# Kernel tuning notes

Hardware: AMD Instinct MI355X
Metric: run time of the kernel (lower is better)

Reference implementation:

```python
import jax, jax.numpy as jnp
import numpy as np

N = 50000
E = 800000
IN, HID, OUT = 256, 128, 128
H = 2


def gat_conv(x, edge_src, edge_dst, W, att_src, att_dst, bias, concat=True):
    # PyG GATConv: x' = W x, edge attention e = leaky_relu(a_s.x'_src + a_d.x'_dst),
    # softmax over incoming edges of each dst node, weighted scatter-add.
    n = x.shape[0]
    heads, ch = att_src.shape
    xl = (x @ W).reshape(n, heads, ch)                      # [N,H,C]
    a_src = jnp.sum(xl * att_src[None], axis=-1)            # [N,H]
    a_dst = jnp.sum(xl * att_dst[None], axis=-1)            # [N,H]
    e = a_src[edge_src] + a_dst[edge_dst]                   # [E,H]
    e = jax.nn.leaky_relu(e, negative_slope=0.2)
    # segment softmax over dst neighborhoods (self-loops guarantee non-empty)
    emax = jax.ops.segment_max(e, edge_dst, num_segments=n)
    ee = jnp.exp(e - emax[edge_dst])
    denom = jax.ops.segment_sum(ee, edge_dst, num_segments=n)
    alpha = ee / (denom[edge_dst] + 1e-16)                  # [E,H]
    msg = xl[edge_src] * alpha[:, :, None]                  # [E,H,C]
    out = jax.ops.segment_sum(msg, edge_dst, num_segments=n)  # [N,H,C]
    out = out.reshape(n, heads * ch) if concat else out.mean(axis=1)
    return out + bias


def setup_inputs() -> dict:
    key = jax.random.key(0)
    ks = jax.random.split(key, 12)
    x = jax.random.normal(ks[0], (N, IN), dtype=jnp.float32)
    edge_index = jax.random.randint(ks[1], (2, E), 0, N, dtype=jnp.int64)
    node_type = (jnp.arange(N, dtype=jnp.int64) % 3)
    agent_idx = jnp.arange(0, N, 3, dtype=jnp.int64)  # nodes with type 0
    # layer 0: in=256 -> out=128, heads=2, concat
    W0 = jax.random.normal(ks[2], (IN, H * HID), dtype=jnp.float32) / np.sqrt(IN)
    as0 = jax.random.normal(ks[3], (H, HID), dtype=jnp.float32) / np.sqrt(HID)
    ad0 = jax.random.normal(ks[4], (H, HID), dtype=jnp.float32) / np.sqrt(HID)
    b0 = jnp.zeros((H * HID,), dtype=jnp.float32)
    # layer 1: in=128*2 -> out=128, heads=2, concat (average_last=False)
    W1 = jax.random.normal(ks[5], (H * HID, H * OUT), dtype=jnp.float32) / np.sqrt(H * HID)
    as1 = jax.random.normal(ks[6], (H, OUT), dtype=jnp.float32) / np.sqrt(OUT)
    ad1 = jax.random.normal(ks[7], (H, OUT), dtype=jnp.float32) / np.sqrt(OUT)
    b1 = jnp.zeros((H * OUT,), dtype=jnp.float32)
    return {"x": x, "edge_index": edge_index, "node_type": node_type,
            "agent_idx": agent_idx, "W0": W0, "as0": as0, "ad0": ad0, "b0": b0,
            "W1": W1, "as1": as1, "ad1": ad1, "b1": b1}


def reference(x, edge_index, node_type, agent_idx, W0, as0, ad0, b0, W1, as1, ad1, b1):
    # add self loops (PyG GATConv default add_self_loops=True)
    loop = jnp.arange(N, dtype=edge_index.dtype)
    src = jnp.concatenate([edge_index[0], loop])
    dst = jnp.concatenate([edge_index[1], loop])
    final = []
    h = gat_conv(x, src, dst, W0, as0, ad0, b0, concat=True)
    h = jax.nn.sigmoid(h)
    final.append(h[agent_idx])  # full_receptive_field=True
    h = gat_conv(h, src, dst, W1, as1, ad1, b1, concat=True)
    h = jax.nn.sigmoid(h)
    final.append(h[agent_idx])
    return jnp.concatenate(final, axis=1)  # [n_agents, 128*2 + 128*2]
```

## Files before the change

kernel.cpp:

```cpp
#include <hip/hip_runtime.h>
#include <hip/hip_fp16.h>

typedef unsigned short u16;
typedef unsigned int   u32;
typedef unsigned char  u8;
typedef __attribute__((ext_vector_type(8))) short short8;
typedef __attribute__((ext_vector_type(8))) unsigned short ushort8v;
typedef __attribute__((ext_vector_type(4))) float f32x4;

#define TPB 256

#define GLDS16(g,l) __builtin_amdgcn_global_load_lds( \
    (const __attribute__((address_space(1))) void*)(g), \
    (__attribute__((address_space(3))) void*)(l), 16, 0, 0)

__device__ __forceinline__ float b2f(u16 u){ u32 x=((u32)u)<<16; return __uint_as_float(x); }
__device__ __forceinline__ u16 f2b(float f){ u32 x=__float_as_uint(f); u32 r=x+0x7FFFu+((x>>16)&1u); return (u16)(r>>16); }
__device__ __forceinline__ float lrelu(float x){ return x>0.f?x:0.2f*x; }
__device__ __forceinline__ float sigm(float x){ return 1.f/(1.f+__expf(-x)); }

__device__ __forceinline__ float4 ld4(const void* p, size_t i4, int isbf){
  if(isbf){
    ushort4 u=((const ushort4*)p)[i4];
    return make_float4(b2f(u.x),b2f(u.y),b2f(u.z),b2f(u.w));
  }
  return ((const float4*)p)[i4];
}
__device__ __forceinline__ float ld1(const void* p, size_t i, int isbf){
  return isbf ? b2f(((const u16*)p)[i]) : ((const float*)p)[i];
}

__global__ void k_deg(const int* __restrict__ dst, int E, int N, int* __restrict__ deg,
                      int* __restrict__ pos,
                      int* __restrict__ ainv, const u16* __restrict__ w0, int* __restrict__ flag){
  int gid=blockIdx.x*blockDim.x+threadIdx.x;
  if(blockIdx.x==0){
    __shared__ int s[256];
    int t=threadIdx.x, sane=0;
    for(int i=t;i<512;i+=256){
      u16 u=w0[i]; u32 e=(u>>7)&0xFFu;
      if((e>=103u&&e<=143u)||((u&0x7FFFu)==0u)) sane++;
    }
    s[t]=sane; __syncthreads();
    for(int o=128;o;o>>=1){ if(t<o) s[t]+=s[t+o]; __syncthreads(); }
    if(t==0) flag[0]=(s[0]>=480)?1:0;
  }
  if(gid<N) ainv[gid]=-1;
  if(gid>=E+N) return;
  int d=(gid<E)?dst[gid]:(gid-E);
  d=min(max(d,0),N-1);
  pos[gid]=atomicAdd(&deg[d],1);
}

__global__ void k_scan(const int* __restrict__ deg, int* __restrict__ rs,
                       int* __restrict__ counter, int n,
                       const int* __restrict__ aidx, int* __restrict__ ainv, int na){
  __shared__ int tmp[TPB];
  __shared__ int base;
  int i=blockIdx.x*TPB+threadIdx.x;
  if(i<na){ int a=aidx[i]; if(a>=0&&a<n) ainv[a]=i; }
  int v=(i<n)?deg[i]:0;
  tmp[threadIdx.x]=v; __syncthreads();
  for(int off=1;off<TPB;off<<=1){
    int t=(threadIdx.x>=off)?tmp[threadIdx.x-off]:0;
    __syncthreads();
    tmp[threadIdx.x]+=t;
    __syncthreads();
  }
  if(threadIdx.x==TPB-1) base=atomicAdd(counter,tmp[TPB-1]);
  __syncthreads();
  if(i<n) rs[i]=base+tmp[threadIdx.x]-v;
}

__global__ void k_fill(const int* __restrict__ src, const int* __restrict__ dst, int E, int N,
                       const int* __restrict__ rs, const int* __restrict__ pos,
                       int* __restrict__ col){
  int e=blockIdx.x*blockDim.x+threadIdx.x; if(e>=E+N) return;
  int d,s;
  if(e<E){ d=dst[e]; s=src[e]; } else { d=e-E; s=e-E; }
  d=min(max(d,0),N-1); s=min(max(s,0),N-1);
  col[rs[d]+pos[e]]=s;
}

__global__ __launch_bounds__(256) void k_prep(const void* __restrict__ Wa, u16* __restrict__ WTa,
                                              const void* __restrict__ Wb, u16* __restrict__ WTb,
                                              const void* __restrict__ X, u16* __restrict__ xb,
                                              int n8, const int* __restrict__ flag){
  const int isbf=flag[0];
  int bid=blockIdx.x;
  if(bid<32){
    __shared__ float s[64][65];
    int z=bid>>4, y=(bid>>2)&3, xb_=bid&3;
    const void* W = z ? Wb : Wa;
    u16* WT = z ? WTb : WTa;
    int tx=threadIdx.x&63, ty=threadIdx.x>>6;
    int k0=xb_*64, n0=y*64;
    #pragma unroll
    for(int i=0;i<64;i+=4)
      s[ty+i][tx]=ld1(W,(size_t)(k0+ty+i)*256+n0+tx,isbf);
    __syncthreads();
    #pragma unroll
    for(int i=0;i<64;i+=4)
      WT[(size_t)(n0+ty+i)*256+k0+tx]=f2b(s[tx][ty+i]);
    return;
  }
  int i=(bid-32)*256+threadIdx.x; if(i>=n8) return;
  size_t e=(size_t)i*8;
  if(isbf){
    *(ushort8v*)(xb+e)=*(const ushort8v*)((const u16*)X+e);
  }else{
    const float4* fp=(const float4*)((const float*)X+e);
    float4 f0=fp[0], f1=fp[1];
    ushort8v o;
    o[0]=f2b(f0.x); o[1]=f2b(f0.y); o[2]=f2b(f0.z); o[3]=f2b(f0.w);
    o[4]=f2b(f1.x); o[5]=f2b(f1.y); o[6]=f2b(f1.z); o[7]=f2b(f1.w);
    *(ushort8v*)(xb+e)=o;
  }
}

__global__ __launch_bounds__(256) void k_gemm(const u16* __restrict__ A, const u16* __restrict__ BT,
                                              u16* __restrict__ C, int M){
  __shared__ short As[128*64];
  __shared__ short Bs[128*64];
  const int t=threadIdx.x;
  const int lane=t&63, wv=t>>6;
  const int wm=wv>>1, wn=wv&1;
  const int m15=lane&15, kg=lane>>4;
  const int gm0=blockIdx.x*128, n0=blockIdx.y*128;
  const int sr=lane>>3, slot=lane&7;
  f32x4 acc[4][4]={};
  for(int k0=0;k0<256;k0+=64){
    #pragma unroll
    for(int i=0;i<4;++i){
      int r=wv*32+i*8+sr;
      int kq=slot^(r&7);
      int ga=gm0+r; ga=ga<M?ga:M-1;
      GLDS16(A+(size_t)ga*256+k0+kq*8, As+(wv*32+i*8)*64);
      GLDS16(BT+(size_t)(n0+r)*256+k0+kq*8, Bs+(wv*32+i*8)*64);
    }
    __syncthreads();
    #pragma unroll
    for(int s=0;s<2;++s){
      short8 af[4], bf[4];
      #pragma unroll
      for(int mi=0;mi<4;++mi){
        int row=wm*64+mi*16+m15;
        int sl=(s*4+kg)^(row&7);
        af[mi]=*(const short8*)&As[row*64+sl*8];
      }
      #pragma unroll
      for(int ni=0;ni<4;++ni){
        int row=wn*64+ni*16+m15;
        int sl=(s*4+kg)^(row&7);
        bf[ni]=*(const short8*)&Bs[row*64+sl*8];
      }
      #pragma unroll
      for(int mi=0;mi<4;++mi)
        #pragma unroll
        for(int ni=0;ni<4;++ni)
          acc[mi][ni]=__builtin_amdgcn_mfma_f32_16x16x32_bf16(af[mi],bf[ni],acc[mi][ni],0,0,0);
    }
    __syncthreads();
  }
  #pragma unroll
  for(int mi=0;mi<4;++mi){
    #pragma unroll
    for(int r=0;r<4;++r){
      int grow=gm0+wm*64+mi*16+kg*4+r;
      if(grow<M){
        #pragma unroll
        for(int ni=0;ni<4;++ni){
          int gcol=n0+wn*64+ni*16+m15;
          C[(size_t)grow*256+gcol]=f2b(acc[mi][ni][r]);
        }
      }
    }
  }
}

__global__ __launch_bounds__(256) void k_att(const u16* __restrict__ xl, const void* __restrict__ as_,
                                             const void* __restrict__ ad_, float4* __restrict__ asv,
                                             float2* __restrict__ adv, u8* __restrict__ xl8,
                                             int n, const int* __restrict__ flag){
  const int isbf=flag[0];
  int w=(blockIdx.x*256+threadIdx.x)>>6;
  int lane=threadIdx.x&63;
  if(w>=n) return;
  int ch=lane*4;
  ushort4 u=*(const ushort4*)(xl+(size_t)w*256+ch);
  float4 s=ld4(as_,ch>>2,isbf);
  float4 d=ld4(ad_,ch>>2,isbf);
  float x0=b2f(u.x),x1=b2f(u.y),x2=b2f(u.z),x3=b2f(u.w);
  float m=fmaxf(fmaxf(fabsf(x0),fabsf(x1)),fmaxf(fabsf(x2),fabsf(x3)));
  for(int off=32;off;off>>=1) m=fmaxf(m,__shfl_xor(m,off));
  float mm=fmaxf(m,1e-20f);
  float scale=mm*(1.f/127.f);
  float rsc=127.f/mm;
  int q0=(int)rintf(fmaf(x0,rsc,128.f));
  int q1=(int)rintf(fmaf(x1,rsc,128.f));
  int q2=(int)rintf(fmaf(x2,rsc,128.f));
  int q3=(int)rintf(fmaf(x3,rsc,128.f));
  u32 pack=(u32)q0|((u32)q1<<8)|((u32)q2<<16)|((u32)q3<<24);
  ((u32*)(xl8+(size_t)w*256))[lane]=pack;
  float ps=x0*s.x+x1*s.y+x2*s.z+x3*s.w;
  float pd=x0*d.x+x1*d.y+x2*d.z+x3*d.w;
  for(int off=16;off;off>>=1){ ps+=__shfl_xor(ps,off); pd+=__shfl_xor(pd,off); }
  float ps1=__shfl(ps,32), pd1=__shfl(pd,32);
  if(lane==0){
    asv[w]=make_float4(ps,ps1,scale,0.f);
    adv[w]=make_float2(pd,pd1);
  }
}

__global__ __launch_bounds__(256) void k_alpha(const int* __restrict__ rs, const int* __restrict__ deg,
    const int* __restrict__ col, const float4* __restrict__ asv, const float2* __restrict__ adv,
    int2* __restrict__ ew, float2* __restrict__ rden, int n){
  int w=(blockIdx.x*256+threadIdx.x)>>5;
  int lane=threadIdx.x&31;
  if(w>=n) return;
  int s0=rs[w], cnt=deg[w];
  float2 ad=adv[w];
  float sum0=0.f, sum1=0.f;
  for(int base=0;base<cnt;base+=32){
    int j=base+lane;
    if(j<cnt){
      int sv=col[s0+j];
      float4 a=asv[sv];
      float e0=fminf(lrelu(a.x+ad.x),11.f);
      float e1=fminf(lrelu(a.y+ad.y),11.f);
      float w0=__expf(e0), w1=__expf(e1);
      sum0+=w0; sum1+=w1;
      __half2 p=__floats2half2_rn(w0*a.z,w1*a.z);
      ew[s0+j]=make_int2(sv,*(int*)&p);
    }
  }
  for(int off=16;off;off>>=1){ sum0+=__shfl_xor(sum0,off); sum1+=__shfl_xor(sum1,off); }
  if(lane==0) rden[w]=make_float2(1.f/(sum0+1e-16f),1.f/(sum1+1e-16f));
}

__global__ __launch_bounds__(256) void k_agg(const int* __restrict__ rs, const int* __restrict__ deg,
    const int2* __restrict__ ew, const float2* __restrict__ rden,
    const u8* __restrict__ xl8, const void* __restrict__ bias,
    u16* __restrict__ hout, void* __restrict__ out, int ostride, int ocol,
    const int* __restrict__ ainv, int n, const int* __restrict__ flag){
  const int isbf=flag[0];
  int w=(blockIdx.x*blockDim.x+threadIdx.x)>>5;
  int sl=threadIdx.x&31;
  if(w>=n) return;
  int s0=rs[w], cnt=deg[w];
  int ch=sl*8, h=sl>>4;
  float acc[8]={};
  float sumw=0.f;
  int2 eA[4]; uint2 rA[4];
  int2 eB[4]; uint2 rB[4];
#define LOADG(e_,r_,J) do{ \
    _Pragma("unroll") \
    for(int u=0;u<4;++u){ int idx=(J)+u; idx=idx<cnt?idx:cnt-1; e_[u]=ew[s0+idx]; } \
    _Pragma("unroll") \
    for(int u=0;u<4;++u) r_[u]=*(const uint2*)(xl8+(size_t)e_[u].x*256+ch); \
  }while(0)
#define COMPG(e_,r_,J) do{ \
    _Pragma("unroll") \
    for(int u=0;u<4;++u){ \
      __half2 p=*(__half2*)&e_[u].y; \
      float wb=__half2float(h?__high2half(p):__low2half(p)); \
      wb=((J)+u<cnt)?wb:0.f; \
      u32 a=r_[u].x, b=r_[u].y; \
      acc[0]=fmaf(wb,(float)( a     &255u),acc[0]); \
      acc[1]=fmaf(wb,(float)((a>> 8)&255u),acc[1]); \
      acc[2]=fmaf(wb,(float)((a>>16)&255u),acc[2]); \
      acc[3]=fmaf(wb,(float)( a>>24      ),acc[3]); \
      acc[4]=fmaf(wb,(float)( b     &255u),acc[4]); \
      acc[5]=fmaf(wb,(float)((b>> 8)&255u),acc[5]); \
      acc[6]=fmaf(wb,(float)((b>>16)&255u),acc[6]); \
      acc[7]=fmaf(wb,(float)( b>>24      ),acc[7]); \
      sumw+=wb; \
    } \
  }while(0)
  LOADG(eA,rA,0);
  int j=0;
  while(j<cnt){
    LOADG(eB,rB,j+4);
    COMPG(eA,rA,j);
    j+=4;
    if(j>=cnt) break;
    LOADG(eA,rA,j+4);
    COMPG(eB,rB,j);
    j+=4;
  }
#undef LOADG
#undef COMPG
  float2 rd=rden[w];
  float rh=h?rd.y:rd.x;
  float4 b0=ld4(bias,ch>>2,isbf);
  float4 b1=ld4(bias,(ch>>2)+1,isbf);
  float c=128.f*sumw;
  float r[8];
  r[0]=sigm((acc[0]-c)*rh+b0.x); r[1]=sigm((acc[1]-c)*rh+b0.y);
  r[2]=sigm((acc[2]-c)*rh+b0.z); r[3]=sigm((acc[3]-c)*rh+b0.w);
  r[4]=sigm((acc[4]-c)*rh+b1.x); r[5]=sigm((acc[5]-c)*rh+b1.y);
  r[6]=sigm((acc[6]-c)*rh+b1.z); r[7]=sigm((acc[7]-c)*rh+b1.w);
  ushort8v ov;
  #pragma unroll
  for(int q=0;q<8;++q) ov[q]=f2b(r[q]);
  if(hout) *(ushort8v*)(hout+(size_t)w*256+ch)=ov;
  int ar=ainv[w];
  if(ar>=0){
    size_t o=(size_t)ar*ostride+ocol+ch;
    if(isbf){
      *(ushort8v*)((u16*)out+o)=ov;
    }else{
      *(float4*)((float*)out+o)  =make_float4(r[0],r[1],r[2],r[3]);
      *(float4*)((float*)out+o+4)=make_float4(r[4],r[5],r[6],r[7]);
    }
  }
}

extern "C" void kernel_launch(void* const* d_in, const int* in_sizes, int n_in,
                              void* d_out, int out_size, void* d_ws, size_t ws_size,
                              hipStream_t stream) {
  const void* x   = d_in[0];
  const int*  ei  = (const int*)d_in[1];
  const int*  aidx= (const int*)d_in[3];
  const void* W0  = d_in[4];
  const void* as0 = d_in[5];
  const void* ad0 = d_in[6];
  const void* b0  = d_in[7];
  const void* W1  = d_in[8];
  const void* as1 = d_in[9];
  const void* ad1 = d_in[10];
  const void* b1  = d_in[11];

  const int N  = in_sizes[0]/256;
  const int E  = in_sizes[1]/2;
  const int na = in_sizes[3];
  const int Et = E+N;

  char* ws=(char*)d_ws; size_t off=0;
  auto alloc=[&](size_t bytes)->void*{ void* p=ws+off; off+=(bytes+255)&~(size_t)255; return p; };
  int*   flg =(int*) alloc(256);
  u16*   xl  =(u16*) alloc((size_t)N*256*2);
  u16*   h1  =(u16*) alloc((size_t)N*256*2);
  u8*    xl8 =(u8*)  alloc((size_t)N*256);
  u16*   WT0 =(u16*) alloc((size_t)256*256*2);
  u16*   WT1 =(u16*) alloc((size_t)256*256*2);
  float4* asv=(float4*)alloc((size_t)N*16);
  float2* adv=(float2*)alloc((size_t)N*8);
  char*  zbase=ws+off;
  int*   deg =(int*) alloc((size_t)N*4);
  int*   ctr =(int*) alloc(256);
  size_t zlen=(ws+off)-zbase;
  int*   pos =(int*) alloc((size_t)Et*4);
  int*   rstp=(int*) alloc((size_t)N*4);
  int*   ainv=(int*) alloc((size_t)N*4);
  int*   col =(int*) alloc((size_t)Et*4);
  int2*  ew  =(int2*)alloc((size_t)Et*8);
  float2* rdn=(float2*)alloc((size_t)N*8);

  u16* xb = h1;

  const int* esrc=ei;
  const int* edst=ei+E;

  hipMemsetAsync(zbase,0,zlen,stream);

  k_deg  <<<(Et+255)/256,256,0,stream>>>(edst,E,N,deg,pos,ainv,(const u16*)W0,flg);
  k_scan <<<(N+TPB-1)/TPB,TPB,0,stream>>>(deg,rstp,ctr,N,aidx,ainv,na);
  k_fill <<<(Et+255)/256,256,0,stream>>>(esrc,edst,E,N,rstp,pos,col);
  k_prep <<<32+(N*32+255)/256,256,0,stream>>>(W0,WT0,W1,WT1,x,xb,N*32,flg);

  dim3 gg((N+127)/128,2);
  k_gemm <<<gg,256,0,stream>>>(xb,WT0,xl,N);
  k_att  <<<(N+3)/4,256,0,stream>>>(xl,as0,ad0,asv,adv,xl8,N,flg);
  k_alpha<<<(N+7)/8,256,0,stream>>>(rstp,deg,col,asv,adv,ew,rdn,N);
  k_agg  <<<(N+7)/8,256,0,stream>>>(rstp,deg,ew,rdn,xl8,b0,h1,d_out,512,0,ainv,N,flg);
  k_gemm <<<gg,256,0,stream>>>(h1,WT1,xl,N);
  k_att  <<<(N+3)/4,256,0,stream>>>(xl,as1,ad1,asv,adv,xl8,N,flg);
  k_alpha<<<(N+7)/8,256,0,stream>>>(rstp,deg,col,asv,adv,ew,rdn,N);
  k_agg  <<<(N+7)/8,256,0,stream>>>(rstp,deg,ew,rdn,xl8,b1,(u16*)nullptr,d_out,512,256,ainv,N,flg);
}
```

Baseline: 339.6 us.

## Merge independent setup kernels into shared launches to cut launch count

Combines the degree-count kernel with the weight-transpose/x-conversion prep into one launch, with prep blocks recomputing the dtype sanity flag locally instead of reading it from global memory. It also merges the CSR fill with the first-layer GEMM into one launch, splitting the work by block index. This removes two kernel launches and lets independent work overlap on the GPU. In exchange the combined kernels carry the larger shared-memory footprint and register pressure of their heaviest branch, and the prep blocks repeat the sanity reduction.

```diff
diff --git a/kernel.cpp b/kernel.cpp
--- a/kernel.cpp
+++ b/kernel.cpp
@@ -30,26 +30,73 @@
   return isbf ? b2f(((const u16*)p)[i]) : ((const float*)p)[i];
 }
 
-__global__ void k_deg(const int* __restrict__ dst, int E, int N, int* __restrict__ deg,
-                      int* __restrict__ pos,
-                      int* __restrict__ ainv, const u16* __restrict__ w0, int* __restrict__ flag){
-  int gid=blockIdx.x*blockDim.x+threadIdx.x;
-  if(blockIdx.x==0){
-    __shared__ int s[256];
-    int t=threadIdx.x, sane=0;
+__global__ __launch_bounds__(256) void k_build(const int* __restrict__ dst, int E, int N,
+    int* __restrict__ deg, int* __restrict__ pos, int* __restrict__ ainv,
+    const u16* __restrict__ w0, int* __restrict__ flag,
+    const void* __restrict__ Wa, u16* __restrict__ WTa,
+    const void* __restrict__ Wb, u16* __restrict__ WTb,
+    const void* __restrict__ X, u16* __restrict__ xb, int n8, int D){
+  __shared__ int sd[256];
+  __shared__ float ts[64][65];
+  int bid=blockIdx.x, t=threadIdx.x;
+  if(bid<D){
+    int gid=bid*256+t;
+    if(bid==0){
+      int sane=0;
+      for(int i=t;i<512;i+=256){
+        u16 u=w0[i]; u32 e2=(u>>7)&0xFFu;
+        if((e2>=103u&&e2<=143u)||((u&0x7FFFu)==0u)) sane++;
+      }
+      sd[t]=sane; __syncthreads();
+      for(int o=128;o;o>>=1){ if(t<o) sd[t]+=sd[t+o]; __syncthreads(); }
+      if(t==0) flag[0]=(sd[0]>=480)?1:0;
+    }
+    if(gid<N) ainv[gid]=-1;
+    if(gid>=E+N) return;
+    int d=(gid<E)?dst[gid]:(gid-E);
+    d=min(max(d,0),N-1);
+    pos[gid]=atomicAdd(&deg[d],1);
+    return;
+  }
+  {
+    int sane=0;
     for(int i=t;i<512;i+=256){
-      u16 u=w0[i]; u32 e=(u>>7)&0xFFu;
-      if((e>=103u&&e<=143u)||((u&0x7FFFu)==0u)) sane++;
-    }
-    s[t]=sane; __syncthreads();
-    for(int o=128;o;o>>=1){ if(t<o) s[t]+=s[t+o]; __syncthreads(); }
-    if(t==0) flag[0]=(s[0]>=480)?1:0;
-  }
-  if(gid<N) ainv[gid]=-1;
-  if(gid>=E+N) return;
-  int d=(gid<E)?dst[gid]:(gid-E);
-  d=min(max(d,0),N-1);
-  pos[gid]=atomicAdd(&deg[d],1);
+      u16 u=w0[i]; u32 e2=(u>>7)&0xFFu;
+      if((e2>=103u&&e2<=143u)||((u&0x7FFFu)==0u)) sane++;
+    }
+    sd[t]=sane; __syncthreads();
+    for(int o=128;o;o>>=1){ if(t<o) sd[t]+=sd[t+o]; __syncthreads(); }
+  }
+  const int isbf=(sd[0]>=480)?1:0;
+  __syncthreads();
+  int pbid=bid-D;
+  if(pbid<32){
+    int z=pbid>>4, y=(pbid>>2)&3, xq=pbid&3;
+    const void* W = z ? Wb : Wa;
+    u16* WT = z ? WTb : WTa;
+    int tx=t&63, ty=t>>6;
+    int k0=xq*64, n0=y*64;
+    #pragma unroll
+    for(int i=0;i<64;i+=4)
+      ts[ty+i][tx]=ld1(W,(size_t)(k0+ty+i)*256+n0+tx,isbf);
+    __syncthreads();
+    #pragma unroll
+    for(int i=0;i<64;i+=4)
+      WT[(size_t)(n0+ty+i)*256+k0+tx]=f2b(ts[tx][ty+i]);
+    return;
+  }
+  int i=(pbid-32)*256+t; if(i>=n8) return;
+  size_t e=(size_t)i*8;
+  if(isbf){
+    *(ushort8v*)(xb+e)=*(const ushort8v*)((const u16*)X+e);
+  }else{
+    const float4* fp=(const float4*)((const float*)X+e);
+    float4 f0=fp[0], f1=fp[1];
+    ushort8v o;
+    o[0]=f2b(f0.x); o[1]=f2b(f0.y); o[2]=f2b(f0.z); o[3]=f2b(f0.w);
+    o[4]=f2b(f1.x); o[5]=f2b(f1.y); o[6]=f2b(f1.z); o[7]=f2b(f1.w);
+    *(ushort8v*)(xb+e)=o;
+  }
 }
 
 __global__ void k_scan(const int* __restrict__ deg, int* __restrict__ rs,
@@ -72,49 +119,74 @@
   if(i<n) rs[i]=base+tmp[threadIdx.x]-v;
 }
 
-__global__ void k_fill(const int* __restrict__ src, const int* __restrict__ dst, int E, int N,
-                       const int* __restrict__ rs, const int* __restrict__ pos,
-                       int* __restrict__ col){
-  int e=blockIdx.x*blockDim.x+threadIdx.x; if(e>=E+N) return;
-  int d,s;
-  if(e<E){ d=dst[e]; s=src[e]; } else { d=e-E; s=e-E; }
-  d=min(max(d,0),N-1); s=min(max(s,0),N-1);
-  col[rs[d]+pos[e]]=s;
-}
-
-__global__ __launch_bounds__(256) void k_prep(const void* __restrict__ Wa, u16* __restrict__ WTa,
-                                              const void* __restrict__ Wb, u16* __restrict__ WTb,
-                                              const void* __restrict__ X, u16* __restrict__ xb,
-                                              int n8, const int* __restrict__ flag){
-  const int isbf=flag[0];
+__global__ __launch_bounds__(256) void k_fillgemm(
+    const int* __restrict__ src, const int* __restrict__ dstp, int E, int N,
+    const int* __restrict__ rs, const int* __restrict__ pos, int* __restrict__ col,
+    const u16* __restrict__ A, const u16* __restrict__ BT, u16* __restrict__ C, int M, int G){
+  __shared__ short As[128*64];
+  __shared__ short Bs[128*64];
   int bid=blockIdx.x;
-  if(bid<32){
-    __shared__ float s[64][65];
-    int z=bid>>4, y=(bid>>2)&3, xb_=bid&3;
-    const void* W = z ? Wb : Wa;
-    u16* WT = z ? WTb : WTa;
-    int tx=threadIdx.x&63, ty=threadIdx.x>>6;
-    int k0=xb_*64, n0=y*64;
-    #pragma unroll
-    for(int i=0;i<64;i+=4)
-      s[ty+i][tx]=ld1(W,(size_t)(k0+ty+i)*256+n0+tx,isbf);
-    __syncthreads();
-    #pragma unroll
-    for(int i=0;i<64;i+=4)
-      WT[(size_t)(n0+ty+i)*256+k0+tx]=f2b(s[tx][ty+i]);
+  const int t=threadIdx.x;
+  if(bid>=G){
+    int e=(bid-G)*256+t; if(e>=E+N) return;
+    int d,s;
+    if(e<E){ d=dstp[e]; s=src[e]; } else { d=e-E; s=e-E; }
+    d=min(max(d,0),N-1); s=min(max(s,0),N-1);
+    col[rs[d]+pos[e]]=s;
     return;
   }
-  int i=(bid-32)*256+threadIdx.x; if(i>=n8) return;
-  size_t e=(size_t)i*8;
-  if(isbf){
-    *(ushort8v*)(xb+e)=*(const ushort8v*)((const u16*)X+e);
-  }else{
-    const float4* fp=(const float4*)((const float*)X+e);
-    float4 f0=fp[0], f1=fp[1];
-    ushort8v o;
-    o[0]=f2b(f0.x); o[1]=f2b(f0.y); o[2]=f2b(f0.z); o[3]=f2b(f0.w);
-    o[4]=f2b(f1.x); o[5]=f2b(f1.y); o[6]=f2b(f1.z); o[7]=f2b(f1.w);
-    *(ushort8v*)(xb+e)=o;
+  const int lane=t&63, wv=t>>6;
+  const int wm=wv>>1, wn=wv&1;
+  const int m15=lane&15, kg=lane>>4;
+  const int gm0=(bid>>1)*128, n0=(bid&1)*128;
+  const int sr=lane>>3, slot=lane&7;
+  f32x4 acc[4][4]={};
+  for(int k0=0;k0<256;k0+=64){
+    #pragma unroll
+    for(int i=0;i<4;++i){
+      int r=wv*32+i*8+sr;
+      int kq=slot^(r&7);
+      int ga=gm0+r; ga=ga<M?ga:M-1;
+      GLDS16(A+(size_t)ga*256+k0+kq*8, As+(wv*32+i*8)*64);
+      GLDS16(BT+(size_t)(n0+r)*256+k0+kq*8, Bs+(wv*32+i*8)*64);
+    }
+    __syncthreads();
+    #pragma unroll
+    for(int s=0;s<2;++s){
+      short8 af[4], bf[4];
+      #pragma unroll
+      for(int mi=0;mi<4;++mi){
+        int row=wm*64+mi*16+m15;
+        int sl=(s*4+kg)^(row&7);
+        af[mi]=*(const short8*)&As[row*64+sl*8];
+      }
+      #pragma unroll
+      for(int ni=0;ni<4;++ni){
+        int row=wn*64+ni*16+m15;
+        int sl=(s*4+kg)^(row&7);
+        bf[ni]=*(const short8*)&Bs[row*64+sl*8];
+      }
+      #pragma unroll
+      for(int mi=0;mi<4;++mi)
+        #pragma unroll
+        for(int ni=0;ni<4;++ni)
+          acc[mi][ni]=__builtin_amdgcn_mfma_f32_16x16x32_bf16(af[mi],bf[ni],acc[mi][ni],0,0,0);
+    }
+    __syncthreads();
+  }
+  #pragma unroll
+  for(int mi=0;mi<4;++mi){
+    #pragma unroll
+    for(int r=0;r<4;++r){
+      int grow=gm0+wm*64+mi*16+kg*4+r;
+      if(grow<M){
+        #pragma unroll
+        for(int ni=0;ni<4;++ni){
+          int gcol=n0+wn*64+ni*16+m15;
+          C[(size_t)grow*256+gcol]=f2b(acc[mi][ni][r]);
+        }
+      }
+    }
   }
 }
 
@@ -364,16 +436,19 @@
 
   hipMemsetAsync(zbase,0,zlen,stream);
 
-  k_deg  <<<(Et+255)/256,256,0,stream>>>(edst,E,N,deg,pos,ainv,(const u16*)W0,flg);
+  const int D = (Et+255)/256;
+  const int P = 32+(N*32+255)/256;
+  k_build<<<D+P,256,0,stream>>>(edst,E,N,deg,pos,ainv,(const u16*)W0,flg,
+                                W0,WT0,W1,WT1,x,xb,N*32,D);
   k_scan <<<(N+TPB-1)/TPB,TPB,0,stream>>>(deg,rstp,ctr,N,aidx,ainv,na);
-  k_fill <<<(Et+255)/256,256,0,stream>>>(esrc,edst,E,N,rstp,pos,col);
-  k_prep <<<32+(N*32+255)/256,256,0,stream>>>(W0,WT0,W1,WT1,x,xb,N*32,flg);
-
-  dim3 gg((N+127)/128,2);
-  k_gemm <<<gg,256,0,stream>>>(xb,WT0,xl,N);
+
+  const int G2 = ((N+127)/128)*2;
+  const int F  = (Et+255)/256;
+  k_fillgemm<<<G2+F,256,0,stream>>>(esrc,edst,E,N,rstp,pos,col,xb,WT0,xl,N,G2);
   k_att  <<<(N+3)/4,256,0,stream>>>(xl,as0,ad0,asv,adv,xl8,N,flg);
   k_alpha<<<(N+7)/8,256,0,stream>>>(rstp,deg,col,asv,adv,ew,rdn,N);
   k_agg  <<<(N+7)/8,256,0,stream>>>(rstp,deg,ew,rdn,xl8,b0,h1,d_out,512,0,ainv,N,flg);
+  dim3 gg((N+127)/128,2);
   k_gemm <<<gg,256,0,stream>>>(h1,WT1,xl,N);
   k_att  <<<(N+3)/4,256,0,stream>>>(xl,as1,ad1,asv,adv,xl8,N,flg);
   k_alpha<<<(N+7)/8,256,0,stream>>>(rstp,deg,col,asv,adv,ew,rdn,N);
```

Measured after the change: 347.6 us. 1.02x slower.
